# Kernel tuning notes

Hardware: AMD Instinct MI355X
Metric: run time of the kernel (lower is better)

Reference implementation:

```python
import jax, jax.numpy as jnp
import numpy as np

DIM = 256
HEADS = 4
HEAD_DIM = DIM // HEADS
SCALE = HEAD_DIM ** -0.5


def setup_inputs() -> dict:
    key = jax.random.key(0)
    k_x, k_wqkv, k_bqkv, k_wp, k_bp = jax.random.split(key, 5)
    B, N = 8, 2048
    x = jax.random.normal(k_x, (B, N, DIM), dtype=jnp.float32)
    # torch nn.Linear weights: [out_features, in_features]
    W_qkv = jax.random.normal(k_wqkv, (3 * DIM, DIM), dtype=jnp.float32) * (DIM ** -0.5)
    b_qkv = jax.random.normal(k_bqkv, (3 * DIM,), dtype=jnp.float32) * 0.02
    W_proj = jax.random.normal(k_wp, (DIM, DIM), dtype=jnp.float32) * (DIM ** -0.5)
    b_proj = jax.random.normal(k_bp, (DIM,), dtype=jnp.float32) * 0.02
    return {"x": x, "W_qkv": W_qkv, "b_qkv": b_qkv, "W_proj": W_proj, "b_proj": b_proj}


def reference(x, W_qkv, b_qkv, W_proj, b_proj):
    B, N, C = x.shape
    h, d = HEADS, HEAD_DIM
    # fused QKV projection: [B,N,3C] -> [3,B,h,N,d]
    qkv = (jnp.einsum('bnc,oc->bno', x, W_qkv) + b_qkv)
    qkv = qkv.reshape(B, N, 3, h, d).transpose(2, 0, 3, 1, 4)
    q, k, v = qkv[0], qkv[1], qkv[2]
    # full N x N score matrix, as in the original module
    attn = jnp.einsum('bhnd,bhmd->bhnm', q, k) * SCALE
    attn = jax.nn.softmax(attn, axis=-1)
    out = jnp.einsum('bhnm,bhmd->bhnd', attn, v)  # [B,h,N,d]
    out = out.transpose(0, 2, 1, 3).reshape(B, N, C)
    return jnp.einsum('bnc,oc->bno', out, W_proj) + b_proj
```

## Files before the change

### kernel.cpp

```cpp
#include <hip/hip_runtime.h>
#include <hip/hip_bf16.h>


typedef __bf16 bf16x8 __attribute__((ext_vector_type(8)));
typedef float f32x4 __attribute__((ext_vector_type(4)));
typedef float f32x16 __attribute__((ext_vector_type(16)));
typedef unsigned u32x2 __attribute__((ext_vector_type(2)));

#define MFMA16(a, b, c) __builtin_amdgcn_mfma_f32_16x16x32_bf16((a), (b), (c), 0, 0, 0)
#define MFMA32(a, b, c) __builtin_amdgcn_mfma_f32_32x32x16_bf16((a), (b), (c), 0, 0, 0)

#define C2 0.18033688011112042f

__device__ __forceinline__ bf16x8 ldg8(const __bf16* p) {
    return *reinterpret_cast<const bf16x8*>(p);
}

__device__ __forceinline__ bf16x8 cvt8(const float* p) {
    const f32x4 a = *reinterpret_cast<const f32x4*>(p);
    const f32x4 b = *reinterpret_cast<const f32x4*>(p + 4);
    bf16x8 r;
    r[0] = (__bf16)a[0]; r[1] = (__bf16)a[1]; r[2] = (__bf16)a[2]; r[3] = (__bf16)a[3];
    r[4] = (__bf16)b[0]; r[5] = (__bf16)b[1]; r[6] = (__bf16)b[2]; r[7] = (__bf16)b[3];
    return r;
}

__device__ __forceinline__ unsigned pk2(float a, float b) {
    __bf16 x = (__bf16)a, y = (__bf16)b;
    unsigned short ux = __builtin_bit_cast(unsigned short, x);
    unsigned short uy = __builtin_bit_cast(unsigned short, y);
    return (unsigned)ux | ((unsigned)uy << 16);
}

__global__ __launch_bounds__(256) void cvt_all(
    const float* __restrict__ X, const float* __restrict__ Wq,
    const float* __restrict__ Wp, __bf16* __restrict__ Xb,
    __bf16* __restrict__ Wqb, __bf16* __restrict__ Wpb)
{
    const int g = blockIdx.x * 256 + threadIdx.x;
    const float* src;
    __bf16* dst;
    int off;
    if (g < 524288)      { src = X;  dst = Xb;  off = g; }
    else if (g < 548864) { src = Wq; dst = Wqb; off = g - 524288; }
    else                 { src = Wp; dst = Wpb; off = g - 548864; }
    *reinterpret_cast<bf16x8*>(dst + (size_t)off * 8) = cvt8(src + (size_t)off * 8);
}

__global__ __launch_bounds__(256) void qkv_gemm(
    const __bf16* __restrict__ X, const __bf16* __restrict__ Wq,
    const float* __restrict__ bq, __bf16* __restrict__ Qw,
    __bf16* __restrict__ Kw, __bf16* __restrict__ Vt)
{
    const int tid = threadIdx.x;
    const int w = tid >> 6, lane = tid & 63;
    const int lo = lane & 15, hi = lane >> 4;
    const int n0 = blockIdx.x * 128;
    const int m0 = blockIdx.y * 128 + w * 32;

    f32x4 acc[2][8] = {};
    const __bf16* xp = X + (m0 + lo) * 256 + hi * 8;
    const __bf16* wp = Wq + (n0 + lo) * 256 + hi * 8;
    #pragma unroll
    for (int k = 0; k < 256; k += 32) {
        bf16x8 a0 = ldg8(xp + k);
        bf16x8 a1 = ldg8(xp + 16 * 256 + k);
        #pragma unroll
        for (int f = 0; f < 8; ++f) {
            bf16x8 bf = ldg8(wp + f * 16 * 256 + k);
            acc[0][f] = MFMA16(a0, bf, acc[0][f]);
            acc[1][f] = MFMA16(a1, bf, acc[1][f]);
        }
    }

    #pragma unroll
    for (int ni = 0; ni < 8; ++ni) {
        const int col = n0 + ni * 16 + lo;
        const float bias = bq[col];
        const float scale = (col < 256) ? C2 : 1.0f;
        #pragma unroll
        for (int mi = 0; mi < 2; ++mi) {
            #pragma unroll
            for (int r = 0; r < 4; ++r) {
                const int row = m0 + mi * 16 + hi * 4 + r;
                const __bf16 hv = (__bf16)((acc[mi][ni][r] + bias) * scale);
                const int bb = row >> 11, n = row & 2047;
                const int d = col & 63;
                if (col < 256) {
                    const int h = col >> 6;
                    Qw[((bb * 4 + h) * 2048 + n) * 64 + d] = hv;
                } else if (col < 512) {
                    const int h = (col - 256) >> 6;
                    Kw[((bb * 4 + h) * 2048 + n) * 64 + d] = hv;
                } else {
                    const int h = (col - 512) >> 6;
                    Vt[((bb * 4 + h) * 64 + d) * 2048 + n] = hv;
                }
            }
        }
    }
}

__global__ __launch_bounds__(512, 4) void attn_kernel(
    const __bf16* __restrict__ Qw, const __bf16* __restrict__ Kw,
    const __bf16* __restrict__ Vt, __bf16* __restrict__ Opart,
    float* __restrict__ Lbuf)
{
    __shared__ __align__(16) char lds[33280];

    const int tid = threadIdx.x;
    const int w = tid >> 6, lane = tid & 63;
    const int l31 = lane & 31, hi5 = lane >> 5;
    const int sw = w & 3;
    const int g  = w >> 2;

    const int bid = blockIdx.x;
    const int work = (bid & 7) * 128 + (bid >> 3);
    const int bh = work >> 5;
    const int split = (work >> 4) & 1;
    const int qx = work & 15;

    const int q = qx * 128 + sw * 32 + l31;
    const int kvbase = split * 1024 + g * 512;
    const int gbase = g * 16384;

    const __bf16* Qp = Qw + (bh * 2048 + q) * 64 + hi5 * 8;
    bf16x8 Qf[4];
    #pragma unroll
    for (int db = 0; db < 4; ++db) Qf[db] = ldg8(Qp + db * 16);

    const __bf16* Kbase = Kw + (size_t)bh * 2048 * 64;
    const __bf16* Vbase = Vt + (size_t)bh * 64 * 2048;

    const int idx = tid & 255;
    const int krow = idx >> 3, kcol8 = (idx & 7) * 8;
    const int swz = ((idx >> 3) & 7) << 4;
    const int kb0 = gbase + ((idx * 16) ^ swz);
    const int kb1 = gbase + (((idx + 256) * 16) ^ swz);
    const int vb0 = gbase + 8192 + ((idx * 16) ^ swz);
    const int vb1 = gbase + 8192 + (((idx + 256) * 16) ^ swz);

    bf16x8 R0 = ldg8(Kbase + (kvbase + krow) * 64 + kcol8);
    bf16x8 R1 = ldg8(Kbase + (kvbase + krow + 32) * 64 + kcol8);
    bf16x8 R2 = ldg8(Vbase + krow * 2048 + kvbase + kcol8);
    bf16x8 R3 = ldg8(Vbase + (krow + 32) * 2048 + kvbase + kcol8);

    f32x16 oacc0 = (f32x16)0.0f, oacc1 = (f32x16)0.0f;
    float lr = 0.0f;

    for (int t = 0; t < 8; ++t) {
        *reinterpret_cast<bf16x8*>(lds + kb0) = R0;
        *reinterpret_cast<bf16x8*>(lds + kb1) = R1;
        *reinterpret_cast<bf16x8*>(lds + vb0) = R2;
        *reinterpret_cast<bf16x8*>(lds + vb1) = R3;
        __syncthreads();

        if (t < 7) {
            const int kv0n = kvbase + (t + 1) * 64;
            R0 = ldg8(Kbase + (kv0n + krow) * 64 + kcol8);
            R1 = ldg8(Kbase + (kv0n + krow + 32) * 64 + kcol8);
            R2 = ldg8(Vbase + krow * 2048 + kv0n + kcol8);
            R3 = ldg8(Vbase + (krow + 32) * 2048 + kv0n + kcol8);
        }

        f32x16 s0 = (f32x16)0.0f, s1 = (f32x16)0.0f;
        #pragma unroll
        for (int db = 0; db < 4; ++db) {
            const int colb = hi5 * 16 + db * 32;
            bf16x8 k0 = *reinterpret_cast<const bf16x8*>(
                lds + gbase + ((l31 * 128 + colb) ^ ((l31 & 7) << 4)));
            bf16x8 k1 = *reinterpret_cast<const bf16x8*>(
                lds + gbase + (((l31 + 32) * 128 + colb) ^ ((l31 & 7) << 4)));
            s0 = MFMA32(k0, Qf[db], s0);
            s1 = MFMA32(k1, Qf[db], s1);
        }

        float p0[16], p1[16];
        #pragma unroll
        for (int i = 0; i < 16; ++i) p0[i] = exp2f(s0[i]);
        #pragma unroll
        for (int i = 0; i < 16; ++i) p1[i] = exp2f(s1[i]);

        float r0 = 0.f, r1 = 0.f, r2 = 0.f, r3 = 0.f;
        #pragma unroll
        for (int i = 0; i < 4; ++i) {
            r0 += p0[i]; r1 += p0[4 + i]; r2 += p0[8 + i]; r3 += p0[12 + i];
            r0 += p1[i]; r1 += p1[4 + i]; r2 += p1[8 + i]; r3 += p1[12 + i];
        }
        lr += (r0 + r1) + (r2 + r3);

#define PVSTEP(PARR, KH)                                                      \
        {                                                                     \
            _Pragma("unroll")                                                 \
            for (int bb2 = 0; bb2 < 2; ++bb2) {                               \
                const int vcolb = KH * 64 + bb2 * 32 + hi5 * 16;              \
                bf16x8 v0 = *reinterpret_cast<const bf16x8*>(                 \
                    lds + gbase + 8192 + ((l31 * 128 + vcolb) ^ ((l31 & 7) << 4))); \
                bf16x8 v1 = *reinterpret_cast<const bf16x8*>(                 \
                    lds + gbase + 8192 + (((l31 + 32) * 128 + vcolb) ^ ((l31 & 7) << 4))); \
                unsigned w0 = pk2(PARR[8 * bb2 + 0], PARR[8 * bb2 + 1]);      \
                unsigned w1 = pk2(PARR[8 * bb2 + 2], PARR[8 * bb2 + 3]);      \
                unsigned w2 = pk2(PARR[8 * bb2 + 4], PARR[8 * bb2 + 5]);      \
                unsigned w3 = pk2(PARR[8 * bb2 + 6], PARR[8 * bb2 + 7]);      \
                asm volatile("v_permlane32_swap_b32 %0, %1" : "+v"(w0), "+v"(w2)); \
                asm volatile("v_permlane32_swap_b32 %0, %1" : "+v"(w1), "+v"(w3)); \
                union { unsigned u[4]; bf16x8 v; } pb;                        \
                pb.u[0] = w0; pb.u[1] = w1; pb.u[2] = w2; pb.u[3] = w3;       \
                oacc0 = MFMA32(v0, pb.v, oacc0);                              \
                oacc1 = MFMA32(v1, pb.v, oacc1);                              \
            }                                                                 \
        }
        PVSTEP(p0, 0)
        PVSTEP(p1, 1)
#undef PVSTEP
        __syncthreads();
    }

    lr += __shfl_xor(lr, 32);

    float* mb = reinterpret_cast<float*>(lds);
    float* lb = reinterpret_cast<float*>(lds + 32768);
    if (g == 1) {
        #pragma unroll
        for (int i = 0; i < 16; ++i) {
            const int r = (i & 3) + 8 * (i >> 2) + 4 * hi5;
            mb[(sw * 64 + r) * 32 + l31] = oacc0[i];
            mb[(sw * 64 + 32 + r) * 32 + l31] = oacc1[i];
        }
        if (hi5 == 0) lb[sw * 32 + l31] = lr;
    }
    __syncthreads();
    if (g == 0) {
        #pragma unroll
        for (int i = 0; i < 16; ++i) {
            const int r = (i & 3) + 8 * (i >> 2) + 4 * hi5;
            oacc0[i] += mb[(sw * 64 + r) * 32 + l31];
            oacc1[i] += mb[(sw * 64 + 32 + r) * 32 + l31];
        }
        lr += lb[sw * 32 + l31];

        __bf16* Od = Opart + ((size_t)(split * 32 + bh) * 2048 + q) * 64 + hi5 * 4;
#define EPI(OACC, DBLK)                                                       \
        {                                                                     \
            _Pragma("unroll")                                                 \
            for (int rq = 0; rq < 4; ++rq) {                                  \
                u32x2 st;                                                     \
                st.x = pk2(OACC[rq * 4 + 0], OACC[rq * 4 + 1]);               \
                st.y = pk2(OACC[rq * 4 + 2], OACC[rq * 4 + 3]);               \
                *reinterpret_cast<u32x2*>(Od + DBLK * 32 + rq * 8) = st;      \
            }                                                                 \
        }
        EPI(oacc0, 0)
        EPI(oacc1, 1)
#undef EPI
        if (hi5 == 0) Lbuf[(size_t)(split * 32 + bh) * 2048 + q] = lr;
    }
}

__global__ __launch_bounds__(256) void merge_kernel(
    const __bf16* __restrict__ Opart, const float* __restrict__ Lbuf,
    __bf16* __restrict__ Ow)
{
    const int g = blockIdx.x * 256 + threadIdx.x;
    const int dg = g & 7;
    const int q = (g >> 3) & 2047;
    const int bh = g >> 14;
    const float l1 = Lbuf[(size_t)bh * 2048 + q];
    const float l2 = Lbuf[(size_t)(32 + bh) * 2048 + q];
    const float inv = 1.0f / (l1 + l2);
    const __bf16* O1 = Opart + ((size_t)bh * 2048 + q) * 64 + dg * 8;
    const __bf16* O2 = O1 + (size_t)32 * 2048 * 64;
    const bf16x8 a = ldg8(O1);
    const bf16x8 b = ldg8(O2);
    bf16x8 r;
    #pragma unroll
    for (int i = 0; i < 8; ++i)
        r[i] = (__bf16)(((float)a[i] + (float)b[i]) * inv);
    const int bb = bh >> 2, h = bh & 3;
    *reinterpret_cast<bf16x8*>(Ow + ((size_t)(bb * 2048 + q)) * 256 + h * 64 + dg * 8) = r;
}

__global__ __launch_bounds__(256) void proj_gemm(
    const __bf16* __restrict__ A, const __bf16* __restrict__ Wp,
    const float* __restrict__ bp, float* __restrict__ out)
{
    const int tid = threadIdx.x;
    const int w = tid >> 6, lane = tid & 63;
    const int lo = lane & 15, hi = lane >> 4;
    const int n0 = blockIdx.x * 128;
    const int m0 = blockIdx.y * 128 + w * 32;

    f32x4 acc[2][8] = {};
    const __bf16* ap = A + (m0 + lo) * 256 + hi * 8;
    const __bf16* wp = Wp + (n0 + lo) * 256 + hi * 8;
    #pragma unroll
    for (int k = 0; k < 256; k += 32) {
        bf16x8 a0 = ldg8(ap + k);
        bf16x8 a1 = ldg8(ap + 16 * 256 + k);
        #pragma unroll
        for (int f = 0; f < 8; ++f) {
            bf16x8 bf = ldg8(wp + f * 16 * 256 + k);
            acc[0][f] = MFMA16(a0, bf, acc[0][f]);
            acc[1][f] = MFMA16(a1, bf, acc[1][f]);
        }
    }
    #pragma unroll
    for (int ni = 0; ni < 8; ++ni) {
        const int col = n0 + ni * 16 + lo;
        const float bias = bp[col];
        #pragma unroll
        for (int mi = 0; mi < 2; ++mi) {
            #pragma unroll
            for (int r = 0; r < 4; ++r) {
                const int row = m0 + mi * 16 + hi * 4 + r;
                out[row * 256 + col] = acc[mi][ni][r] + bias;
            }
        }
    }
}

extern "C" void kernel_launch(void* const* d_in, const int* in_sizes, int n_in,
                              void* d_out, int out_size, void* d_ws, size_t ws_size,
                              hipStream_t stream)
{
    const float* x  = (const float*)d_in[0];
    const float* Wq = (const float*)d_in[1];
    const float* bq = (const float*)d_in[2];
    const float* Wp = (const float*)d_in[3];
    const float* bp = (const float*)d_in[4];

    __bf16* ws = (__bf16*)d_ws;
    const size_t SZ = (size_t)32 * 2048 * 64;
    __bf16* Xb  = ws;
    __bf16* Wqb = Xb + SZ;
    __bf16* Wpb = Wqb + 196608;
    __bf16* Qw  = Wpb + 65536;
    __bf16* Kw  = Qw + SZ;
    __bf16* Vt  = Kw + SZ;
    float*  Lbuf = (float*)(Vt + SZ);
    __bf16* Ow  = Xb;

    __bf16* Opart = (__bf16*)d_out;

    cvt_all<<<2176, 256, 0, stream>>>(x, Wq, Wp, Xb, Wqb, Wpb);
    qkv_gemm<<<dim3(6, 128), 256, 0, stream>>>(Xb, Wqb, bq, Qw, Kw, Vt);
    attn_kernel<<<1024, 512, 0, stream>>>(Qw, Kw, Vt, Opart, Lbuf);
    merge_kernel<<<2048, 256, 0, stream>>>(Opart, Lbuf, Ow);
    proj_gemm<<<dim3(2, 128), 256, 0, stream>>>(Ow, Wpb, bp, (float*)d_out);
}
```

Measured before the change: 147.5 us.

## Fold KV split into larger attention blocks and drop merge kernel

The attention kernel now launches 512 blocks of 1024 threads, with four warp-groups each covering a quarter of the KV range for one query tile. Their partial outputs are reduced in shared memory as a bf16 tree, and the softmax normalization is applied in the epilogue. This removes the separate merge kernel along with its partial-output and Lbuf round trips through global memory. In exchange, blocks double in size and use more LDS, the grid is halved, which may lower occupancy, and the reduction adds bf16 rounding of the partial sums.

```diff
diff --git a/kernel.cpp b/kernel.cpp
--- a/kernel.cpp
+++ b/kernel.cpp
@@ -101,12 +101,11 @@
     }
 }
 
-__global__ __launch_bounds__(512, 4) void attn_kernel(
+__global__ __launch_bounds__(1024, 2) void attn_kernel(
     const __bf16* __restrict__ Qw, const __bf16* __restrict__ Kw,
-    const __bf16* __restrict__ Vt, __bf16* __restrict__ Opart,
-    float* __restrict__ Lbuf)
-{
-    __shared__ __align__(16) char lds[33280];
+    const __bf16* __restrict__ Vt, __bf16* __restrict__ Ow)
+{
+    __shared__ __align__(16) char lds[65536];
 
     const int tid = threadIdx.x;
     const int w = tid >> 6, lane = tid & 63;
@@ -115,13 +114,12 @@
     const int g  = w >> 2;
 
     const int bid = blockIdx.x;
-    const int work = (bid & 7) * 128 + (bid >> 3);
-    const int bh = work >> 5;
-    const int split = (work >> 4) & 1;
+    const int work = (bid & 7) * 64 + (bid >> 3);
+    const int bh = work >> 4;
     const int qx = work & 15;
 
     const int q = qx * 128 + sw * 32 + l31;
-    const int kvbase = split * 1024 + g * 512;
+    const int kvbase = g * 512;
     const int gbase = g * 16384;
 
     const __bf16* Qp = Qw + (bh * 2048 + q) * 64 + hi5 * 8;
@@ -218,66 +216,59 @@
 
     lr += __shfl_xor(lr, 32);
 
-    float* mb = reinterpret_cast<float*>(lds);
-    float* lb = reinterpret_cast<float*>(lds + 32768);
-    if (g == 1) {
-        #pragma unroll
-        for (int i = 0; i < 16; ++i) {
-            const int r = (i & 3) + 8 * (i >> 2) + 4 * hi5;
-            mb[(sw * 64 + r) * 32 + l31] = oacc0[i];
-            mb[(sw * 64 + 32 + r) * 32 + l31] = oacc1[i];
-        }
-        if (hi5 == 0) lb[sw * 32 + l31] = lr;
-    }
+    __bf16* mb = reinterpret_cast<__bf16*>(lds);
+    float*  lb = reinterpret_cast<float*>(lds + 32768);
+    const int half = g >> 1;
+    const int abase = half * 8192;
+
+#define MWRITE(BASE, LIDX)                                                    \
+    {                                                                         \
+        _Pragma("unroll")                                                     \
+        for (int i = 0; i < 16; ++i) {                                        \
+            const int r = (i & 3) + 8 * (i >> 2) + 4 * hi5;                   \
+            mb[(BASE) + (sw * 64 + r) * 32 + l31] = (__bf16)oacc0[i];         \
+            mb[(BASE) + (sw * 64 + 32 + r) * 32 + l31] = (__bf16)oacc1[i];    \
+        }                                                                     \
+        if (hi5 == 0) lb[(LIDX) * 128 + sw * 32 + l31] = lr;                  \
+    }
+#define MACC(BASE, LIDX)                                                      \
+    {                                                                         \
+        _Pragma("unroll")                                                     \
+        for (int i = 0; i < 16; ++i) {                                        \
+            const int r = (i & 3) + 8 * (i >> 2) + 4 * hi5;                   \
+            oacc0[i] += (float)mb[(BASE) + (sw * 64 + r) * 32 + l31];         \
+            oacc1[i] += (float)mb[(BASE) + (sw * 64 + 32 + r) * 32 + l31];    \
+        }                                                                     \
+        lr += lb[(LIDX) * 128 + sw * 32 + l31];                               \
+    }
+
+    if (g & 1) MWRITE(abase, half);
+    __syncthreads();
+    if (!(g & 1)) MACC(abase, half);
+    __syncthreads();
+    if (g == 2) MWRITE(0, 0);
     __syncthreads();
     if (g == 0) {
-        #pragma unroll
-        for (int i = 0; i < 16; ++i) {
-            const int r = (i & 3) + 8 * (i >> 2) + 4 * hi5;
-            oacc0[i] += mb[(sw * 64 + r) * 32 + l31];
-            oacc1[i] += mb[(sw * 64 + 32 + r) * 32 + l31];
-        }
-        lr += lb[sw * 32 + l31];
-
-        __bf16* Od = Opart + ((size_t)(split * 32 + bh) * 2048 + q) * 64 + hi5 * 4;
+        MACC(0, 0);
+        const float invl = 1.0f / lr;
+        const int bb = bh >> 2, h = bh & 3;
+        __bf16* Op = Ow + ((size_t)(bb * 2048 + q)) * 256 + h * 64 + hi5 * 4;
 #define EPI(OACC, DBLK)                                                       \
         {                                                                     \
             _Pragma("unroll")                                                 \
             for (int rq = 0; rq < 4; ++rq) {                                  \
                 u32x2 st;                                                     \
-                st.x = pk2(OACC[rq * 4 + 0], OACC[rq * 4 + 1]);               \
-                st.y = pk2(OACC[rq * 4 + 2], OACC[rq * 4 + 3]);               \
-                *reinterpret_cast<u32x2*>(Od + DBLK * 32 + rq * 8) = st;      \
+                st.x = pk2(OACC[rq * 4 + 0] * invl, OACC[rq * 4 + 1] * invl); \
+                st.y = pk2(OACC[rq * 4 + 2] * invl, OACC[rq * 4 + 3] * invl); \
+                *reinterpret_cast<u32x2*>(Op + DBLK * 32 + rq * 8) = st;      \
             }                                                                 \
         }
         EPI(oacc0, 0)
         EPI(oacc1, 1)
 #undef EPI
-        if (hi5 == 0) Lbuf[(size_t)(split * 32 + bh) * 2048 + q] = lr;
-    }
-}
-
-__global__ __launch_bounds__(256) void merge_kernel(
-    const __bf16* __restrict__ Opart, const float* __restrict__ Lbuf,
-    __bf16* __restrict__ Ow)
-{
-    const int g = blockIdx.x * 256 + threadIdx.x;
-    const int dg = g & 7;
-    const int q = (g >> 3) & 2047;
-    const int bh = g >> 14;
-    const float l1 = Lbuf[(size_t)bh * 2048 + q];
-    const float l2 = Lbuf[(size_t)(32 + bh) * 2048 + q];
-    const float inv = 1.0f / (l1 + l2);
-    const __bf16* O1 = Opart + ((size_t)bh * 2048 + q) * 64 + dg * 8;
-    const __bf16* O2 = O1 + (size_t)32 * 2048 * 64;
-    const bf16x8 a = ldg8(O1);
-    const bf16x8 b = ldg8(O2);
-    bf16x8 r;
-    #pragma unroll
-    for (int i = 0; i < 8; ++i)
-        r[i] = (__bf16)(((float)a[i] + (float)b[i]) * inv);
-    const int bb = bh >> 2, h = bh & 3;
-    *reinterpret_cast<bf16x8*>(Ow + ((size_t)(bb * 2048 + q)) * 256 + h * 64 + dg * 8) = r;
+    }
+#undef MWRITE
+#undef MACC
 }
 
 __global__ __launch_bounds__(256) void proj_gemm(
@@ -337,14 +328,10 @@
     __bf16* Qw  = Wpb + 65536;
     __bf16* Kw  = Qw + SZ;
     __bf16* Vt  = Kw + SZ;
-    float*  Lbuf = (float*)(Vt + SZ);
     __bf16* Ow  = Xb;
-
-    __bf16* Opart = (__bf16*)d_out;
 
     cvt_all<<<2176, 256, 0, stream>>>(x, Wq, Wp, Xb, Wqb, Wpb);
     qkv_gemm<<<dim3(6, 128), 256, 0, stream>>>(Xb, Wqb, bq, Qw, Kw, Vt);
-    attn_kernel<<<1024, 512, 0, stream>>>(Qw, Kw, Vt, Opart, Lbuf);
-    merge_kernel<<<2048, 256, 0, stream>>>(Opart, Lbuf, Ow);
+    attn_kernel<<<512, 1024, 0, stream>>>(Qw, Kw, Vt, Ow);
     proj_gemm<<<dim3(2, 128), 256, 0, stream>>>(Ow, Wpb, bp, (float*)d_out);
 }
```

After: 142.9 us. 1.03x faster.
